# Kernel optimization log

Measured on AMD Instinct MI355X. Metric: run time of the kernel, lower is better.

The kernel has to match this reference:

```python
import jax, jax.numpy as jnp
import numpy as np

EMBED = 1024
HEADS = 16
HEAD_DIM = EMBED // HEADS
FFN = 4 * EMBED
LN_EPS = 1e-5


def _layernorm(x, g, b):
    mu = jnp.mean(x, axis=-1, keepdims=True)
    var = jnp.var(x, axis=-1, keepdims=True)
    return (x - mu) * jax.lax.rsqrt(var + LN_EPS) * g + b


def setup_inputs() -> dict:
    key = jax.random.key(0)
    ks = jax.random.split(key, 12)
    s = 0.02
    return {
        "x": jax.random.normal(ks[0], (2, 2048, EMBED), dtype=jnp.float32),
        "Wq": jax.random.normal(ks[1], (HEAD_DIM, HEAD_DIM), dtype=jnp.float32) * s,
        "Wk": jax.random.normal(ks[2], (HEAD_DIM, HEAD_DIM), dtype=jnp.float32) * s,
        "Wv": jax.random.normal(ks[3], (HEAD_DIM, HEAD_DIM), dtype=jnp.float32) * s,
        "Wo": jax.random.normal(ks[4], (EMBED, EMBED), dtype=jnp.float32) * s,
        "bo": jnp.zeros((EMBED,), dtype=jnp.float32),
        "ln1_g": jnp.ones((EMBED,), dtype=jnp.float32),
        "ln1_b": jnp.zeros((EMBED,), dtype=jnp.float32),
        "ln2_g": jnp.ones((EMBED,), dtype=jnp.float32),
        "ln2_b": jnp.zeros((EMBED,), dtype=jnp.float32),
        "W1": jax.random.normal(ks[5], (FFN, EMBED), dtype=jnp.float32) * s,
        "b1": jnp.zeros((FFN,), dtype=jnp.float32),
        "W2": jax.random.normal(ks[6], (EMBED, FFN), dtype=jnp.float32) * s,
        "b2": jnp.zeros((EMBED,), dtype=jnp.float32),
    }


def reference(x, Wq, Wk, Wv, Wo, bo, ln1_g, ln1_b, ln2_g, ln2_b, W1, b1, W2, b2):
    N, S, E = x.shape
    xh = x.reshape(N, S, HEADS, HEAD_DIM)  # [n, s, h, d]
    # shared per-head_dim projections (nn.Linear without bias: x @ W.T)
    q = jnp.einsum('nshd,ed->nshe', xh, Wq)
    k = jnp.einsum('nshd,ed->nshe', xh, Wk)
    v = jnp.einsum('nshd,ed->nshe', xh, Wv)
    # NOTE: original scales by sqrt(embed_size), not sqrt(head_dim)
    energy = jnp.einsum('nqhd,nkhd->nhqk', q, k) / jnp.sqrt(jnp.float32(E))
    attn = jax.nn.softmax(energy, axis=-1)
    ctx = jnp.einsum('nhqk,nkhd->nqhd', attn, v).reshape(N, S, E)
    attn_out = ctx @ Wo.T + bo
    x1 = _layernorm(attn_out + x, ln1_g, ln1_b)
    ff = jax.nn.relu(x1 @ W1.T + b1) @ W2.T + b2
    out = _layernorm(ff + x1, ln2_g, ln2_b)  # dropout p=0 (eval) -> identity
    return out
```

## Files before the change

### kernel.cpp

```cpp
#include <hip/hip_runtime.h>
#include <hip/hip_bf16.h>

#define TOKENS 4096
#define EMB    1024
#define SEQ    2048
#define NHEAD  16
#define HDIM   64
#define FFN_D  4096

typedef __attribute__((ext_vector_type(8))) short bf16x8;
typedef __attribute__((ext_vector_type(4))) float f32x4;
typedef __attribute__((ext_vector_type(2))) float f32x2;
typedef __attribute__((ext_vector_type(16))) float f32x16;
typedef __attribute__((ext_vector_type(4))) unsigned int u32x4;
typedef __attribute__((ext_vector_type(2))) unsigned int u32x2;

static __device__ __forceinline__ unsigned short f2bf(float f) {
  unsigned int u = __float_as_uint(f);
  unsigned int r = (u + 0x7fffu + ((u >> 16) & 1u)) >> 16;
  return (unsigned short)r;
}

static __device__ __forceinline__ float bf2f(unsigned short b) {
  return __uint_as_float(((unsigned int)b) << 16);
}

static __device__ __forceinline__ unsigned int pk2(float a, float b) {
  __hip_bfloat162 h = __float22bfloat162_rn(float2{a, b});
  return *reinterpret_cast<unsigned int*>(&h);
}

static __device__ __forceinline__ f32x2 pk_fma(f32x2 a, f32x2 b, f32x2 c) {
  f32x2 d;
  asm("v_pk_fma_f32 %0, %1, %2, %3" : "=v"(d) : "v"(a), "v"(b), "v"(c));
  return d;
}
static __device__ __forceinline__ f32x2 pk_add(f32x2 a, f32x2 b) {
  f32x2 d;
  asm("v_pk_add_f32 %0, %1, %2" : "=v"(d) : "v"(a), "v"(b));
  return d;
}

static __device__ __forceinline__ int xcd_swz(int lid, int nwg) {
  int q = nwg >> 3, r = nwg & 7;
  int xcd = lid & 7, off = lid >> 3;
  return (xcd < r ? xcd * (q + 1) : r * (q + 1) + (xcd - r) * q) + off;
}

static __device__ __forceinline__ void gload_lds16(const unsigned short* g,
                                                   unsigned short* l) {
  __builtin_amdgcn_global_load_lds(
      (const __attribute__((address_space(1))) void*)g,
      (__attribute__((address_space(3))) void*)l, 16, 0, 0);
}

__global__ __launch_bounds__(256) void cvt3_kernel(
    const float* __restrict__ Wo, const float* __restrict__ W1,
    const float* __restrict__ W2, const float* __restrict__ Wq,
    const float* __restrict__ Wk, const float* __restrict__ Wv,
    unsigned short* __restrict__ Wob, unsigned short* __restrict__ W1b,
    unsigned short* __restrict__ W2b, unsigned short* __restrict__ Wqb,
    unsigned short* __restrict__ Wkb, unsigned short* __restrict__ Wvb) {
  const int M = 1024 * 1024;
  int i = (blockIdx.x * 256 + threadIdx.x) * 8;
  const float* src;
  unsigned short* dst;
  int off;
  float scale = 1.0f;
  if (i < M) { src = Wo; dst = Wob; off = i; }
  else if (i < 5 * M) { src = W1; dst = W1b; off = i - M; }
  else if (i < 9 * M) { src = W2; dst = W2b; off = i - 5 * M; }
  else if (i < 9 * M + 4096) {
    src = Wq; dst = Wqb; off = i - 9 * M; scale = 0.045111751f;
  }
  else if (i < 9 * M + 8192) { src = Wk; dst = Wkb; off = i - 9 * M - 4096; }
  else { src = Wv; dst = Wvb; off = i - 9 * M - 8192; }
  float4 v0 = *reinterpret_cast<const float4*>(&src[off]);
  float4 v1 = *reinterpret_cast<const float4*>(&src[off + 4]);
  bf16x8 ov;
  ov[0] = (short)f2bf(v0.x * scale); ov[1] = (short)f2bf(v0.y * scale);
  ov[2] = (short)f2bf(v0.z * scale); ov[3] = (short)f2bf(v0.w * scale);
  ov[4] = (short)f2bf(v1.x * scale); ov[5] = (short)f2bf(v1.y * scale);
  ov[6] = (short)f2bf(v1.z * scale); ov[7] = (short)f2bf(v1.w * scale);
  *reinterpret_cast<bf16x8*>(&dst[off]) = ov;
}

__global__ __launch_bounds__(256) void qkv_mfma(
    const float* __restrict__ x,
    const unsigned short* __restrict__ Wqb, const unsigned short* __restrict__ Wkb,
    const unsigned short* __restrict__ Wvb,
    unsigned short* __restrict__ q, unsigned short* __restrict__ k,
    unsigned short* __restrict__ vT) {
  __shared__ unsigned short Xs[64][72];
  __shared__ unsigned short Wqs[64][72], Wks[64][72], Wvs[64][72];
  const int tid = threadIdx.x;
  const int w = tid >> 6, lane = tid & 63;
  const int lg = lane >> 4, lc = lane & 15;
  const int b = blockIdx.x;
  const int T0 = (b >> 4) * 64;
  const int h = b & 15;
  const int n = T0 >> 11;
  const int s0 = T0 & 2047;

  #pragma unroll
  for (int it = 0; it < 4; it++) {
    int idx = it * 256 + tid;
    int row = idx >> 4, c4 = (idx & 15) * 4;
    float4 xv = *reinterpret_cast<const float4*>(
        &x[(size_t)(T0 + row) * EMB + h * 64 + c4]);
    uint2 pw = {pk2(xv.x, xv.y), pk2(xv.z, xv.w)};
    *reinterpret_cast<uint2*>(&Xs[row][c4]) = pw;
  }
  #pragma unroll
  for (int it = 0; it < 4; it++) {
    int idx = it * 256 + tid;
    int e = idx >> 4, c4 = (idx & 15) * 4;
    *reinterpret_cast<uint2*>(&Wqs[e][c4]) =
        *reinterpret_cast<const uint2*>(&Wqb[e * 64 + c4]);
    *reinterpret_cast<uint2*>(&Wks[e][c4]) =
        *reinterpret_cast<const uint2*>(&Wkb[e * 64 + c4]);
    *reinterpret_cast<uint2*>(&Wvs[e][c4]) =
        *reinterpret_cast<const uint2*>(&Wvb[e * 64 + c4]);
  }
  __syncthreads();

  bf16x8 xf0 = *reinterpret_cast<const bf16x8*>(&Xs[w * 16 + lc][lg * 8]);
  bf16x8 xf1 = *reinterpret_cast<const bf16x8*>(&Xs[w * 16 + lc][32 + lg * 8]);

  f32x4 aq[4], ak[4], av[4];
  #pragma unroll
  for (int eg = 0; eg < 4; eg++) {
    f32x4 z = {0.f, 0.f, 0.f, 0.f};
    aq[eg] = z; ak[eg] = z; av[eg] = z;
  }

  #pragma unroll
  for (int eg = 0; eg < 4; eg++) {
    bf16x8 wq0 = *reinterpret_cast<const bf16x8*>(&Wqs[eg * 16 + lc][lg * 8]);
    bf16x8 wq1 = *reinterpret_cast<const bf16x8*>(&Wqs[eg * 16 + lc][32 + lg * 8]);
    bf16x8 wk0 = *reinterpret_cast<const bf16x8*>(&Wks[eg * 16 + lc][lg * 8]);
    bf16x8 wk1 = *reinterpret_cast<const bf16x8*>(&Wks[eg * 16 + lc][32 + lg * 8]);
    bf16x8 wv0 = *reinterpret_cast<const bf16x8*>(&Wvs[eg * 16 + lc][lg * 8]);
    bf16x8 wv1 = *reinterpret_cast<const bf16x8*>(&Wvs[eg * 16 + lc][32 + lg * 8]);
    aq[eg] = __builtin_amdgcn_mfma_f32_16x16x32_bf16(wq0, xf0, aq[eg], 0, 0, 0);
    aq[eg] = __builtin_amdgcn_mfma_f32_16x16x32_bf16(wq1, xf1, aq[eg], 0, 0, 0);
    ak[eg] = __builtin_amdgcn_mfma_f32_16x16x32_bf16(wk0, xf0, ak[eg], 0, 0, 0);
    ak[eg] = __builtin_amdgcn_mfma_f32_16x16x32_bf16(wk1, xf1, ak[eg], 0, 0, 0);
    av[eg] = __builtin_amdgcn_mfma_f32_16x16x32_bf16(xf0, wv0, av[eg], 0, 0, 0);
    av[eg] = __builtin_amdgcn_mfma_f32_16x16x32_bf16(xf1, wv1, av[eg], 0, 0, 0);
  }

  const size_t qoff = (size_t)(T0 + w * 16 + lc) * EMB + h * 64;
  #pragma unroll
  for (int eg = 0; eg < 4; eg++) {
    uint2 pq = {pk2(aq[eg][0], aq[eg][1]), pk2(aq[eg][2], aq[eg][3])};
    uint2 pkk = {pk2(ak[eg][0], ak[eg][1]), pk2(ak[eg][2], ak[eg][3])};
    *reinterpret_cast<uint2*>(&q[qoff + eg * 16 + lg * 4]) = pq;
    *reinterpret_cast<uint2*>(&k[qoff + eg * 16 + lg * 4]) = pkk;
  }
  const size_t vtb = (size_t)(n * 16 + h) * 64 * SEQ;
  #pragma unroll
  for (int eg = 0; eg < 4; eg++) {
    uint2 pv = {pk2(av[eg][0], av[eg][1]), pk2(av[eg][2], av[eg][3])};
    *reinterpret_cast<uint2*>(
        &vT[vtb + (size_t)(eg * 16 + lc) * SEQ + s0 + w * 16 + lg * 4]) = pv;
  }
}

__global__ __launch_bounds__(256) void attn_mfma(
    const unsigned short* __restrict__ qg, const unsigned short* __restrict__ kg,
    const unsigned short* __restrict__ vtg, unsigned short* __restrict__ ctx) {
  __shared__ unsigned short Ks[2][8192];
  __shared__ unsigned short Vt[2][8192];
  const int tid = threadIdx.x;
  const int w = tid >> 6, lane = tid & 63;
  const int l31 = lane & 31, h5 = lane >> 5;
  const int q7 = l31 & 7;
  const int swzV = l31 & 15;
  const int b = xcd_swz(blockIdx.x, 512);
  const int qt = b & 15, nh = b >> 4;
  const int n = nh >> 4, h = nh & 15;
  const size_t base = (size_t)n * SEQ * EMB + h * 64;
  const size_t vtbase = (size_t)(n * 16 + h) * 64 * SEQ;
  const int q0 = qt * 128 + w * 32;
  const int NT = SEQ / 128;

  bf16x8 qa[4];
  #pragma unroll
  for (int t = 0; t < 4; t++)
    qa[t] = *reinterpret_cast<const bf16x8*>(
        &qg[base + (size_t)(q0 + l31) * EMB + 16 * t + 8 * h5]);

  f32x16 o0 = {}, o1 = {};
  f32x2 l2 = {0.f, 0.f};

  auto stage = [&](int bi, int t) {
    const int j0 = t * 128;
    #pragma unroll
    for (int rnd = 0; rnd < 4; rnd++) {
      const int glbase = rnd * 256 + w * 64;
      const int gl = glbase + lane;
      {
        const int row = gl >> 3, gp = gl & 7;
        const int gsrc = (gp ^ (row & 7)) * 8;
        gload_lds16(&kg[base + (size_t)(j0 + row) * EMB + gsrc], &Ks[bi][glbase * 8]);
      }
      {
        const int row = gl >> 4, gp = gl & 15;
        const int gsrc = (gp ^ (row & 15)) * 8;
        gload_lds16(&vtg[vtbase + (size_t)row * SEQ + j0 + gsrc], &Vt[bi][glbase * 8]);
      }
    }
  };

  const f32x2 PC0 = {0.2402265069f, 0.2402265069f};
  const f32x2 PC1 = {0.6931471806f, 0.6931471806f};
  const f32x2 PONE = {1.0f, 1.0f};

  stage(0, 0);
  #pragma unroll 1
  for (int t = 0; t < NT; ++t) {
    if (t + 1 < NT) {
      stage((t + 1) & 1, t + 1);
      asm volatile("s_waitcnt vmcnt(8)" ::: "memory");
    } else {
      asm volatile("s_waitcnt vmcnt(0)" ::: "memory");
    }
    __builtin_amdgcn_sched_barrier(0);
    __builtin_amdgcn_s_barrier();
    __builtin_amdgcn_sched_barrier(0);

    const unsigned short* KsB = &Ks[t & 1][0];
    const unsigned short* VtB = &Vt[t & 1][0];

    f32x16 s0 = {}, s1 = {}, s2 = {}, s3 = {};
    auto qk = [&](f32x16& sv, int sb) {
      #pragma unroll
      for (int tt = 0; tt < 4; tt++) {
        const int g = 2 * tt + h5;
        bf16x8 ka = *reinterpret_cast<const bf16x8*>(
            &KsB[(sb * 32 + l31) * 64 + (g ^ q7) * 8]);
        sv = __builtin_amdgcn_mfma_f32_32x32x16_bf16(ka, qa[tt], sv, 0, 0, 0);
      }
    };
    __builtin_amdgcn_s_setprio(1);
    qk(s0, 0); qk(s1, 1); qk(s2, 2); qk(s3, 3);
    __builtin_amdgcn_s_setprio(0);

    auto ex = [&](f32x16& sv) {
      f32x2* p = reinterpret_cast<f32x2*>(&sv);
      #pragma unroll
      for (int r = 0; r < 8; r++) {
        f32x2 x = p[r];
        f32x2 tt = pk_fma(x, PC0, PC1);
        f32x2 e = pk_fma(x, tt, PONE);
        p[r] = e;
        l2 = pk_add(l2, e);
      }
    };
    ex(s0); ex(s1); ex(s2); ex(s3);

    auto pv = [&](f32x16& sv, int sb) {
      #pragma unroll
      for (int tb = 0; tb < 2; tb++) {
        unsigned W0 = pk2(sv[8 * tb + 0], sv[8 * tb + 1]);
        unsigned W1 = pk2(sv[8 * tb + 2], sv[8 * tb + 3]);
        unsigned W2 = pk2(sv[8 * tb + 4], sv[8 * tb + 5]);
        unsigned W3 = pk2(sv[8 * tb + 6], sv[8 * tb + 7]);
        u32x2 r02 = __builtin_amdgcn_permlane32_swap(W0, W2, false, false);
        u32x2 r13 = __builtin_amdgcn_permlane32_swap(W1, W3, false, false);
        u32x4 pv4 = {r02[0], r13[0], r02[1], r13[1]};
        bf16x8 pbt = *reinterpret_cast<bf16x8*>(&pv4);
        const int kg2 = 2 * (2 * sb + tb) + h5;
        bf16x8 va0 = *reinterpret_cast<const bf16x8*>(
            &VtB[l31 * 128 + (kg2 ^ swzV) * 8]);
        bf16x8 va1 = *reinterpret_cast<const bf16x8*>(
            &VtB[(32 + l31) * 128 + (kg2 ^ swzV) * 8]);
        o0 = __builtin_amdgcn_mfma_f32_32x32x16_bf16(va0, pbt, o0, 0, 0, 0);
        o1 = __builtin_amdgcn_mfma_f32_32x32x16_bf16(va1, pbt, o1, 0, 0, 0);
      }
    };
    __builtin_amdgcn_s_setprio(1);
    pv(s0, 0); pv(s1, 1); pv(s2, 2); pv(s3, 3);
    __builtin_amdgcn_s_setprio(0);

    if (t + 1 < NT) {
      __builtin_amdgcn_sched_barrier(0);
      __builtin_amdgcn_s_barrier();
    }
  }

  float lh = l2[0] + l2[1];
  unsigned pb = __float_as_uint(lh);
  u32x2 pr = __builtin_amdgcn_permlane32_swap(pb, pb, false, false);
  const float rl = 1.0f / (__uint_as_float(pr[0]) + __uint_as_float(pr[1]));

  const size_t orow = base + (size_t)(q0 + l31) * EMB;
  #pragma unroll
  for (int s = 0; s < 2; s++) {
    #pragma unroll
    for (int rg = 0; rg < 4; rg++) {
      float v0 = (s ? o1[4 * rg]     : o0[4 * rg])     * rl;
      float v1 = (s ? o1[4 * rg + 1] : o0[4 * rg + 1]) * rl;
      float v2 = (s ? o1[4 * rg + 2] : o0[4 * rg + 2]) * rl;
      float v3 = (s ? o1[4 * rg + 3] : o0[4 * rg + 3]) * rl;
      const int d0 = 8 * rg + 4 * h5 + 32 * s;
      uint2 pw = {pk2(v0, v1), pk2(v2, v3)};
      *reinterpret_cast<uint2*>(&ctx[orow + d0]) = pw;
    }
  }
}

template <int K, bool RELU, bool RES, bool OBF, bool BIAS>
__global__ __launch_bounds__(256) void gemm_mfma(
    const unsigned short* __restrict__ X, const unsigned short* __restrict__ W,
    const float* __restrict__ bias, const float* __restrict__ resid,
    void* __restrict__ outp, int Nout, int ldk) {
  __shared__ unsigned short As[128 * 64];
  __shared__ unsigned short Bs[128 * 64];
  const int tid = threadIdx.x;
  const int w = tid >> 6, lane = tid & 63;
  const int lg = lane >> 4, lc = lane & 15;
  const int wr = w >> 1, wc = w & 1;
  const int nx = gridDim.x, ny = gridDim.y;
  const int nwg = nx * ny * gridDim.z;
  const int lid = blockIdx.x + nx * (blockIdx.y + ny * blockIdx.z);
  const int swz = xcd_swz(lid, nwg);
  const int bx = swz % nx, by = (swz / nx) % ny, bz = swz / (nx * ny);
  const int c0 = bx * 128, t0 = by * 128;
  const int koff = bz * K;

  f32x4 acc[4][4];
  #pragma unroll
  for (int m = 0; m < 4; m++)
    #pragma unroll
    for (int n = 0; n < 4; n++) {
      f32x4 z = {0.f, 0.f, 0.f, 0.f};
      acc[m][n] = z;
    }

  for (int i0 = 0; i0 < K; i0 += 64) {
    __syncthreads();
    #pragma unroll
    for (int rnd = 0; rnd < 4; rnd++) {
      const int glbase = rnd * 256 + w * 64;
      const int gl = glbase + lane;
      const int row = gl >> 3, gp = gl & 7;
      const int gsrc = (gp ^ (row & 7)) * 8;
      gload_lds16(&X[(size_t)(t0 + row) * ldk + koff + i0 + gsrc], &As[glbase * 8]);
      gload_lds16(&W[(size_t)(c0 + row) * ldk + koff + i0 + gsrc], &Bs[glbase * 8]);
    }
    __syncthreads();
    #pragma unroll
    for (int kk = 0; kk < 2; kk++) {
      bf16x8 a[4], b[4];
      #pragma unroll
      for (int m = 0; m < 4; m++) {
        const int R = wr * 64 + m * 16 + lc;
        a[m] = *reinterpret_cast<const bf16x8*>(
            &As[R * 64 + ((kk * 4 + lg) ^ (R & 7)) * 8]);
      }
      #pragma unroll
      for (int n = 0; n < 4; n++) {
        const int R = wc * 64 + n * 16 + lc;
        b[n] = *reinterpret_cast<const bf16x8*>(
            &Bs[R * 64 + ((kk * 4 + lg) ^ (R & 7)) * 8]);
      }
      #pragma unroll
      for (int m = 0; m < 4; m++)
        #pragma unroll
        for (int n = 0; n < 4; n++)
          acc[m][n] = __builtin_amdgcn_mfma_f32_16x16x32_bf16(a[m], b[n], acc[m][n], 0, 0, 0);
    }
  }

  const size_t zoff = (size_t)bz * ((size_t)TOKENS * Nout);
  float* outf = (float*)outp;
  unsigned short* outb = (unsigned short*)outp;
  #pragma unroll
  for (int m = 0; m < 4; m++) {
    #pragma unroll
    for (int r = 0; r < 4; r++) {
      int row = t0 + wr * 64 + m * 16 + lg * 4 + r;
      #pragma unroll
      for (int n = 0; n < 4; n++) {
        int col = c0 + wc * 64 + n * 16 + lc;
        float val = acc[m][n][r];
        if constexpr (BIAS) val += bias[col];
        if constexpr (RES) val += resid[(size_t)row * Nout + col];
        if constexpr (RELU) val = fmaxf(val, 0.f);
        if constexpr (OBF) outb[zoff + (size_t)row * Nout + col] = f2bf(val);
        else outf[zoff + (size_t)row * Nout + col] = val;
      }
    }
  }
}

__global__ __launch_bounds__(256) void ln1_fuse(
    const unsigned short* __restrict__ pW, const float* __restrict__ bo,
    const float* __restrict__ x, const float* __restrict__ g,
    const float* __restrict__ b, unsigned short* __restrict__ ob) {
  __shared__ float sw[4], ssw[4];
  const int tid = threadIdx.x;
  const int row = blockIdx.x;
  const int wave = tid >> 6, lane = tid & 63;
  const size_t TE = (size_t)TOKENS * EMB;
  const size_t idx = (size_t)row * EMB + tid * 4;
  uint2 u0 = *reinterpret_cast<const uint2*>(&pW[idx]);
  uint2 u1 = *reinterpret_cast<const uint2*>(&pW[idx + TE]);
  float4 xv = *reinterpret_cast<const float4*>(&x[idx]);
  float4 bb = *reinterpret_cast<const float4*>(&bo[tid * 4]);
  const unsigned short* p0 = (const unsigned short*)&u0;
  const unsigned short* p1 = (const unsigned short*)&u1;
  float v[4];
  v[0] = bf2f(p0[0]) + bf2f(p1[0]) + bb.x + xv.x;
  v[1] = bf2f(p0[1]) + bf2f(p1[1]) + bb.y + xv.y;
  v[2] = bf2f(p0[2]) + bf2f(p1[2]) + bb.z + xv.z;
  v[3] = bf2f(p0[3]) + bf2f(p1[3]) + bb.w + xv.w;
  float s = v[0] + v[1] + v[2] + v[3];
  float ss = v[0] * v[0] + v[1] * v[1] + v[2] * v[2] + v[3] * v[3];
  #pragma unroll
  for (int off = 32; off >= 1; off >>= 1) {
    s += __shfl_xor(s, off, 64);
    ss += __shfl_xor(ss, off, 64);
  }
  if (lane == 0) { sw[wave] = s; ssw[wave] = ss; }
  __syncthreads();
  float st = sw[0] + sw[1] + sw[2] + sw[3];
  float sst = ssw[0] + ssw[1] + ssw[2] + ssw[3];
  float mu = st * (1.f / EMB);
  float var = sst * (1.f / EMB) - mu * mu;
  float rs = rsqrtf(var + 1e-5f);
  float4 gv = *reinterpret_cast<const float4*>(&g[tid * 4]);
  float4 bv = *reinterpret_cast<const float4*>(&b[tid * 4]);
  float r0 = (v[0] - mu) * rs * gv.x + bv.x;
  float r1 = (v[1] - mu) * rs * gv.y + bv.y;
  float r2 = (v[2] - mu) * rs * gv.z + bv.z;
  float r3 = (v[3] - mu) * rs * gv.w + bv.w;
  uint2 pw = {pk2(r0, r1), pk2(r2, r3)};
  *reinterpret_cast<uint2*>(&ob[idx]) = pw;
}

__global__ __launch_bounds__(256) void ln2_fuse(
    const unsigned short* __restrict__ pc, const float* __restrict__ b2,
    const unsigned short* __restrict__ x1b, const float* __restrict__ g,
    const float* __restrict__ b, float* __restrict__ out) {
  __shared__ float sw[4], ssw[4];
  const int tid = threadIdx.x;
  const int row = blockIdx.x;
  const int wave = tid >> 6, lane = tid & 63;
  const size_t TE = (size_t)TOKENS * EMB;
  const size_t idx = (size_t)row * EMB + tid * 4;
  uint2 u0 = *reinterpret_cast<const uint2*>(&pc[idx]);
  uint2 u1 = *reinterpret_cast<const uint2*>(&pc[idx + TE]);
  uint2 u2 = *reinterpret_cast<const uint2*>(&x1b[idx]);
  float4 bb = *reinterpret_cast<const float4*>(&b2[tid * 4]);
  const unsigned short* p0 = (const unsigned short*)&u0;
  const unsigned short* p1 = (const unsigned short*)&u1;
  const unsigned short* p2 = (const unsigned short*)&u2;
  float v[4];
  v[0] = bf2f(p0[0]) + bf2f(p1[0]) + bb.x + bf2f(p2[0]);
  v[1] = bf2f(p0[1]) + bf2f(p1[1]) + bb.y + bf2f(p2[1]);
  v[2] = bf2f(p0[2]) + bf2f(p1[2]) + bb.z + bf2f(p2[2]);
  v[3] = bf2f(p0[3]) + bf2f(p1[3]) + bb.w + bf2f(p2[3]);
  float s = v[0] + v[1] + v[2] + v[3];
  float ss = v[0] * v[0] + v[1] * v[1] + v[2] * v[2] + v[3] * v[3];
  #pragma unroll
  for (int off = 32; off >= 1; off >>= 1) {
    s += __shfl_xor(s, off, 64);
    ss += __shfl_xor(ss, off, 64);
  }
  if (lane == 0) { sw[wave] = s; ssw[wave] = ss; }
  __syncthreads();
  float st = sw[0] + sw[1] + sw[2] + sw[3];
  float sst = ssw[0] + ssw[1] + ssw[2] + ssw[3];
  float mu = st * (1.f / EMB);
  float var = sst * (1.f / EMB) - mu * mu;
  float rs = rsqrtf(var + 1e-5f);
  float4 gv = *reinterpret_cast<const float4*>(&g[tid * 4]);
  float4 bv = *reinterpret_cast<const float4*>(&b[tid * 4]);
  float4 res;
  res.x = (v[0] - mu) * rs * gv.x + bv.x;
  res.y = (v[1] - mu) * rs * gv.y + bv.y;
  res.z = (v[2] - mu) * rs * gv.z + bv.z;
  res.w = (v[3] - mu) * rs * gv.w + bv.w;
  *reinterpret_cast<float4*>(&out[idx]) = res;
}

extern "C" void kernel_launch(void* const* d_in, const int* in_sizes, int n_in,
                              void* d_out, int out_size, void* d_ws, size_t ws_size,
                              hipStream_t stream) {
  const float* x    = (const float*)d_in[0];
  const float* Wq   = (const float*)d_in[1];
  const float* Wk   = (const float*)d_in[2];
  const float* Wv   = (const float*)d_in[3];
  const float* Wo   = (const float*)d_in[4];
  const float* bo   = (const float*)d_in[5];
  const float* ln1g = (const float*)d_in[6];
  const float* ln1b = (const float*)d_in[7];
  const float* ln2g = (const float*)d_in[8];
  const float* ln2b = (const float*)d_in[9];
  const float* W1   = (const float*)d_in[10];
  const float* b1   = (const float*)d_in[11];
  const float* W2   = (const float*)d_in[12];
  const float* b2   = (const float*)d_in[13];
  float* out = (float*)d_out;

  const size_t TE = (size_t)TOKENS * EMB;
  const size_t MB = 1024 * 1024;
  unsigned short* qb  = (unsigned short*)d_ws;
  unsigned short* kb  = qb + TE;
  unsigned short* vT  = kb + TE;
  unsigned short* ctx = vT + TE;
  unsigned short* pW  = (unsigned short*)((char*)d_ws + 32 * MB);
  unsigned short* x1b = (unsigned short*)((char*)d_ws + 48 * MB);
  unsigned short* ff1 = (unsigned short*)d_ws;
  unsigned short* pC  = (unsigned short*)((char*)d_ws + 32 * MB);
  unsigned short* Wob = (unsigned short*)((char*)d_ws + 56 * MB);
  unsigned short* W1b = (unsigned short*)((char*)d_ws + 58 * MB);
  unsigned short* W2b = (unsigned short*)((char*)d_ws + 66 * MB);
  unsigned short* Wqb = (unsigned short*)((char*)d_ws + 74 * MB);
  unsigned short* Wkb = Wqb + 4096;
  unsigned short* Wvb = Wkb + 4096;

  cvt3_kernel<<<(9 * 1024 * 1024 + 12288) / 2048, 256, 0, stream>>>(
      Wo, W1, W2, Wq, Wk, Wv, Wob, W1b, W2b, Wqb, Wkb, Wvb);

  qkv_mfma<<<(TOKENS / 64) * NHEAD, 256, 0, stream>>>(x, Wqb, Wkb, Wvb, qb, kb, vT);
  attn_mfma<<<512, 256, 0, stream>>>(qb, kb, vT, ctx);
  gemm_mfma<512, false, false, true, false>
      <<<dim3(EMB / 128, TOKENS / 128, 2), 256, 0, stream>>>(ctx, Wob, nullptr, nullptr, pW, EMB, 1024);
  ln1_fuse<<<TOKENS, 256, 0, stream>>>(pW, bo, x, ln1g, ln1b, x1b);
  gemm_mfma<1024, true, false, true, true>
      <<<dim3(FFN_D / 128, TOKENS / 128), 256, 0, stream>>>(x1b, W1b, b1, nullptr, ff1, FFN_D, 1024);
  gemm_mfma<2048, false, false, true, false>
      <<<dim3(EMB / 128, TOKENS / 128, 2), 256, 0, stream>>>(ff1, W2b, nullptr, nullptr, pC, EMB, 4096);
  ln2_fuse<<<TOKENS, 256, 0, stream>>>(pC, b2, x1b, ln2g, ln2b, out);
}
```

Measured before the change: 190.6 us.

## Overlap weight bf16 conversion with attention via extra blocks; remap FFN1 tiles

Drops the standalone conversion of Wo, W1 and W2 and runs it in 128 extra workgroups appended to the attention launch. The aim is to hide the memory-bound conversion behind the compute-bound attention instead of paying for it serially. The small Q/K/V weight conversion stays in a tiny kernel of its own. The FFN1 GEMM gets a custom XCD-aware tile mapping that groups nearby tiles per XCD for L2 reuse. The risk is that the extra blocks contend with attention for CU slots and bandwidth, or lengthen its tail.

```diff
diff --git a/kernel.cpp b/kernel.cpp
--- a/kernel.cpp
+++ b/kernel.cpp
@@ -54,27 +54,18 @@
       (__attribute__((address_space(3))) void*)l, 16, 0, 0);
 }
 
-__global__ __launch_bounds__(256) void cvt3_kernel(
-    const float* __restrict__ Wo, const float* __restrict__ W1,
-    const float* __restrict__ W2, const float* __restrict__ Wq,
-    const float* __restrict__ Wk, const float* __restrict__ Wv,
-    unsigned short* __restrict__ Wob, unsigned short* __restrict__ W1b,
-    unsigned short* __restrict__ W2b, unsigned short* __restrict__ Wqb,
+__global__ __launch_bounds__(256) void cvt_qkv(
+    const float* __restrict__ Wq, const float* __restrict__ Wk,
+    const float* __restrict__ Wv, unsigned short* __restrict__ Wqb,
     unsigned short* __restrict__ Wkb, unsigned short* __restrict__ Wvb) {
-  const int M = 1024 * 1024;
   int i = (blockIdx.x * 256 + threadIdx.x) * 8;
   const float* src;
   unsigned short* dst;
   int off;
   float scale = 1.0f;
-  if (i < M) { src = Wo; dst = Wob; off = i; }
-  else if (i < 5 * M) { src = W1; dst = W1b; off = i - M; }
-  else if (i < 9 * M) { src = W2; dst = W2b; off = i - 5 * M; }
-  else if (i < 9 * M + 4096) {
-    src = Wq; dst = Wqb; off = i - 9 * M; scale = 0.045111751f;
-  }
-  else if (i < 9 * M + 8192) { src = Wk; dst = Wkb; off = i - 9 * M - 4096; }
-  else { src = Wv; dst = Wvb; off = i - 9 * M - 8192; }
+  if (i < 4096) { src = Wq; dst = Wqb; off = i; scale = 0.045111751f; }
+  else if (i < 8192) { src = Wk; dst = Wkb; off = i - 4096; }
+  else { src = Wv; dst = Wvb; off = i - 8192; }
   float4 v0 = *reinterpret_cast<const float4*>(&src[off]);
   float4 v1 = *reinterpret_cast<const float4*>(&src[off + 4]);
   bf16x8 ov;
@@ -169,10 +160,39 @@
 
 __global__ __launch_bounds__(256) void attn_mfma(
     const unsigned short* __restrict__ qg, const unsigned short* __restrict__ kg,
-    const unsigned short* __restrict__ vtg, unsigned short* __restrict__ ctx) {
+    const unsigned short* __restrict__ vtg, unsigned short* __restrict__ ctx,
+    const float* __restrict__ Wo, const float* __restrict__ W1,
+    const float* __restrict__ W2, unsigned short* __restrict__ Wob,
+    unsigned short* __restrict__ W1b, unsigned short* __restrict__ W2b) {
   __shared__ unsigned short Ks[2][8192];
   __shared__ unsigned short Vt[2][8192];
   const int tid = threadIdx.x;
+
+  if (blockIdx.x >= 512) {
+    const int cb = blockIdx.x - 512;
+    const int M = 1024 * 1024;
+    #pragma unroll 1
+    for (int it = 0; it < 36; ++it) {
+      int unit = cb + 128 * it;
+      int i = unit * 2048 + tid * 8;
+      const float* src;
+      unsigned short* dst;
+      int off;
+      if (i < M) { src = Wo; dst = Wob; off = i; }
+      else if (i < 5 * M) { src = W1; dst = W1b; off = i - M; }
+      else { src = W2; dst = W2b; off = i - 5 * M; }
+      float4 v0 = *reinterpret_cast<const float4*>(&src[off]);
+      float4 v1 = *reinterpret_cast<const float4*>(&src[off + 4]);
+      bf16x8 ov;
+      ov[0] = (short)f2bf(v0.x); ov[1] = (short)f2bf(v0.y);
+      ov[2] = (short)f2bf(v0.z); ov[3] = (short)f2bf(v0.w);
+      ov[4] = (short)f2bf(v1.x); ov[5] = (short)f2bf(v1.y);
+      ov[6] = (short)f2bf(v1.z); ov[7] = (short)f2bf(v1.w);
+      *reinterpret_cast<bf16x8*>(&dst[off]) = ov;
+    }
+    return;
+  }
+
   const int w = tid >> 6, lane = tid & 63;
   const int l31 = lane & 31, h5 = lane >> 5;
   const int q7 = l31 & 7;
@@ -264,11 +284,11 @@
       #pragma unroll
       for (int tb = 0; tb < 2; tb++) {
         unsigned W0 = pk2(sv[8 * tb + 0], sv[8 * tb + 1]);
-        unsigned W1 = pk2(sv[8 * tb + 2], sv[8 * tb + 3]);
-        unsigned W2 = pk2(sv[8 * tb + 4], sv[8 * tb + 5]);
+        unsigned W1v = pk2(sv[8 * tb + 2], sv[8 * tb + 3]);
+        unsigned W2v = pk2(sv[8 * tb + 4], sv[8 * tb + 5]);
         unsigned W3 = pk2(sv[8 * tb + 6], sv[8 * tb + 7]);
-        u32x2 r02 = __builtin_amdgcn_permlane32_swap(W0, W2, false, false);
-        u32x2 r13 = __builtin_amdgcn_permlane32_swap(W1, W3, false, false);
+        u32x2 r02 = __builtin_amdgcn_permlane32_swap(W0, W2v, false, false);
+        u32x2 r13 = __builtin_amdgcn_permlane32_swap(W1v, W3, false, false);
         u32x4 pv4 = {r02[0], r13[0], r02[1], r13[1]};
         bf16x8 pbt = *reinterpret_cast<bf16x8*>(&pv4);
         const int kg2 = 2 * (2 * sb + tb) + h5;
@@ -325,8 +345,16 @@
   const int nx = gridDim.x, ny = gridDim.y;
   const int nwg = nx * ny * gridDim.z;
   const int lid = blockIdx.x + nx * (blockIdx.y + ny * blockIdx.z);
-  const int swz = xcd_swz(lid, nwg);
-  const int bx = swz % nx, by = (swz / nx) % ny, bz = swz / (nx * ny);
+  int bx, by, bz;
+  if (nx == 32 && ny == 32 && gridDim.z == 1) {
+    const int kx = lid & 7, off = lid >> 3;
+    bx = (kx & 1) * 16 + (off & 15);
+    by = (kx >> 1) * 8 + (off >> 4);
+    bz = 0;
+  } else {
+    const int swz = xcd_swz(lid, nwg);
+    bx = swz % nx; by = (swz / nx) % ny; bz = swz / (nx * ny);
+  }
   const int c0 = bx * 128, t0 = by * 128;
   const int koff = bz * K;
 
@@ -523,11 +551,9 @@
   unsigned short* Wkb = Wqb + 4096;
   unsigned short* Wvb = Wkb + 4096;
 
-  cvt3_kernel<<<(9 * 1024 * 1024 + 12288) / 2048, 256, 0, stream>>>(
-      Wo, W1, W2, Wq, Wk, Wv, Wob, W1b, W2b, Wqb, Wkb, Wvb);
-
+  cvt_qkv<<<6, 256, 0, stream>>>(Wq, Wk, Wv, Wqb, Wkb, Wvb);
   qkv_mfma<<<(TOKENS / 64) * NHEAD, 256, 0, stream>>>(x, Wqb, Wkb, Wvb, qb, kb, vT);
-  attn_mfma<<<512, 256, 0, stream>>>(qb, kb, vT, ctx);
+  attn_mfma<<<640, 256, 0, stream>>>(qb, kb, vT, ctx, Wo, W1, W2, Wob, W1b, W2b);
   gemm_mfma<512, false, false, true, false>
       <<<dim3(EMB / 128, TOKENS / 128, 2), 256, 0, stream>>>(ctx, Wob, nullptr, nullptr, pW, EMB, 1024);
   ln1_fuse<<<TOKENS, 256, 0, stream>>>(pW, bo, x, ln1g, ln1b, x1b);
```

New measurement: 195.7 us. +2.7%, slower.
